# Performance work log

Measured on AMD Instinct MI355X. Metric: run time of the kernel, lower is better.

## Reference

```python
import jax, jax.numpy as jnp
import numpy as np

DIM = 1024
SEQ_LEN = 4096
K = 256
HEADS = 16
DIM_HEAD = DIM // HEADS  # 64
BATCH = 4


def setup_inputs() -> dict:
    key = jax.random.key(0)
    ks = jax.random.split(key, 8)
    x = jax.random.normal(ks[0], (BATCH, SEQ_LEN, DIM), dtype=jnp.float32)
    # nn.Linear weights are [out, in]; y = x @ W.T
    std_lin = 1.0 / np.sqrt(DIM)
    Wq = jax.random.uniform(ks[1], (HEADS * DIM_HEAD, DIM), minval=-std_lin, maxval=std_lin, dtype=jnp.float32)
    Wk = jax.random.uniform(ks[2], (HEADS * DIM_HEAD, DIM), minval=-std_lin, maxval=std_lin, dtype=jnp.float32)
    Wv = jax.random.uniform(ks[3], (HEADS * DIM_HEAD, DIM), minval=-std_lin, maxval=std_lin, dtype=jnp.float32)
    # proj_k/proj_v init_: uniform(-1/sqrt(k), 1/sqrt(k)) on [seq_len, k]
    std_p = 1.0 / np.sqrt(K)
    proj_k = jax.random.uniform(ks[4], (SEQ_LEN, K), minval=-std_p, maxval=std_p, dtype=jnp.float32)
    proj_v = jax.random.uniform(ks[5], (SEQ_LEN, K), minval=-std_p, maxval=std_p, dtype=jnp.float32)
    std_o = 1.0 / np.sqrt(HEADS * DIM_HEAD)
    Wo = jax.random.uniform(ks[6], (DIM, HEADS * DIM_HEAD), minval=-std_o, maxval=std_o, dtype=jnp.float32)
    bo = jax.random.uniform(ks[7], (DIM,), minval=-std_o, maxval=std_o, dtype=jnp.float32)
    return {"x": x, "Wq": Wq, "Wk": Wk, "Wv": Wv, "proj_k": proj_k, "proj_v": proj_v, "Wo": Wo, "bo": bo}


def reference(x, Wq, Wk, Wv, proj_k, proj_v, Wo, bo):
    b, n, d = x.shape
    h, dh, k = HEADS, DIM_HEAD, K
    # q/k/v projections
    q = jnp.einsum('bnd,ed->bne', x, Wq)            # [b, n, h*dh]
    keys = jnp.einsum('bnd,ed->bne', x, Wk)         # [b, n, h*dh]
    vals = jnp.einsum('bnd,ed->bne', x, Wv)         # [b, n, h*dh]
    # low-rank projection along sequence: [b, n, e] x [n, k] -> [b, k, e]
    keys = jnp.einsum('bne,nk->bke', keys, proj_k[:n])
    vals = jnp.einsum('bne,nk->bke', vals, proj_v[:n])
    # split heads
    q = q.reshape(b, n, h, dh).transpose(0, 2, 1, 3)        # [b, h, n, dh]
    keys = keys.reshape(b, k, h, dh).transpose(0, 2, 1, 3)  # [b, h, k, dh]
    vals = vals.reshape(b, k, h, dh).transpose(0, 2, 1, 3)  # [b, h, k, dh]
    dots = jnp.einsum('bhnd,bhkd->bhnk', q, keys) * (dh ** -0.5)
    attn = jax.nn.softmax(dots, axis=-1)
    out = jnp.einsum('bhnk,bhkd->bhnd', attn, vals)
    out = out.transpose(0, 2, 1, 3).reshape(b, n, h * dh)
    return jnp.einsum('bne,oe->bno', out, Wo) + bo
```

## Files before the change

### kernel.cpp

```cpp
#include <hip/hip_runtime.h>
#include <hip/hip_bf16.h>
#include <stdint.h>

typedef unsigned short u16;
typedef __attribute__((ext_vector_type(8))) short bf16x8;
typedef __attribute__((ext_vector_type(4))) float f32x4;

#define DEV __device__ __forceinline__

DEV u16 f2bf(float f) {
  union { float f; unsigned u; } v; v.f = f;
  unsigned r = (v.u + 0x7fffu + ((v.u >> 16) & 1u)) >> 16;
  return (u16)r;
}

DEV float bf2f(u16 h) {
  union { unsigned u; float f; } v; v.u = ((unsigned)h) << 16;
  return v.f;
}

DEV unsigned pk2(float lo, float hi) {
  union { __hip_bfloat162 h; unsigned u; } c;
  c.h = __float22bfloat162_rn(make_float2(lo, hi));
  return c.u;
}

DEV f32x4 mfma16(bf16x8 a, bf16x8 b, f32x4 c) {
  return __builtin_amdgcn_mfma_f32_16x16x32_bf16(a, b, c, 0, 0, 0);
}

DEV void gload_lds16(const u16* g, u16* l) {
  __builtin_amdgcn_global_load_lds((const __attribute__((address_space(1))) void*)g,
                                   (__attribute__((address_space(3))) void*)l, 16, 0, 0);
}

#define QSCALE 0.18033688011112042f

__global__ void cvt_xpose_kernel(const float* __restrict__ src, u16* __restrict__ dst_rm,
                                 u16* __restrict__ dst_tp, int R, int C,
                                 long zS, long zRM, long zTP) {
  __shared__ u16 tile[64][72];
  src += (size_t)blockIdx.z * zS;
  dst_tp += (size_t)blockIdx.z * zTP;
  int r0 = blockIdx.y * 64, c0 = blockIdx.x * 64;
  int tr = threadIdx.x >> 2, tc = (threadIdx.x & 3) * 16;
  const float* s = src + (size_t)(r0 + tr) * C + c0 + tc;
  u16 loc[16];
#pragma unroll
  for (int q = 0; q < 4; ++q) {
    float4 v = ((const float4*)s)[q];
    loc[q * 4 + 0] = f2bf(v.x); loc[q * 4 + 1] = f2bf(v.y);
    loc[q * 4 + 2] = f2bf(v.z); loc[q * 4 + 3] = f2bf(v.w);
  }
#pragma unroll
  for (int i = 0; i < 16; ++i) tile[tr][tc + i] = loc[i];
  if (dst_rm) {
    u16* d = dst_rm + (size_t)blockIdx.z * zRM + (size_t)(r0 + tr) * C + c0 + tc;
    *(bf16x8*)d = *(const bf16x8*)&loc[0];
    *(bf16x8*)(d + 8) = *(const bf16x8*)&loc[8];
  }
  __syncthreads();
  u16 tmp[16];
#pragma unroll
  for (int i = 0; i < 16; ++i) tmp[i] = tile[tc + i][tr];
  u16* d = dst_tp + (size_t)(c0 + tr) * R + r0 + tc;
  *(bf16x8*)d = *(const bf16x8*)&tmp[0];
  *(bf16x8*)(d + 8) = *(const bf16x8*)&tmp[8];
}

__global__ void cvt_misc_kernel(const float* __restrict__ s0, const float* __restrict__ s1,
                                const float* __restrict__ s2, const float* __restrict__ s3,
                                u16* __restrict__ d0, u16* __restrict__ d1,
                                u16* __restrict__ d2, u16* __restrict__ d3,
                                const float* __restrict__ pk, const float* __restrict__ pv,
                                u16* __restrict__ projT) {
  __shared__ u16 tile[64][72];
  const int y = blockIdx.y;
  if (y < 4) {
    const float* s; u16* d;
    switch (y) {
      case 0: s = s0; d = d0; break;
      case 1: s = s1; d = d1; break;
      case 2: s = s2; d = d2; break;
      default: s = s3; d = d3; break;
    }
    int i = blockIdx.x * 256 + threadIdx.x;
    float4 v = ((const float4*)s)[i];
    ushort4 o; o.x = f2bf(v.x); o.y = f2bf(v.y); o.z = f2bf(v.z); o.w = f2bf(v.w);
    ((ushort4*)d)[i] = o;
    return;
  }
  if (blockIdx.x >= 256) return;
  const float* src = (y == 4) ? pk : pv;
  u16* dst = projT + (size_t)(y - 4) * 1048576;
  int r0 = (blockIdx.x >> 2) * 64, c0 = (blockIdx.x & 3) * 64;
  int tr = threadIdx.x >> 2, tc = (threadIdx.x & 3) * 16;
  const float* s = src + (size_t)(r0 + tr) * 256 + c0 + tc;
  u16 loc[16];
#pragma unroll
  for (int q = 0; q < 4; ++q) {
    float4 v = ((const float4*)s)[q];
    loc[q * 4 + 0] = f2bf(v.x); loc[q * 4 + 1] = f2bf(v.y);
    loc[q * 4 + 2] = f2bf(v.z); loc[q * 4 + 3] = f2bf(v.w);
  }
#pragma unroll
  for (int i = 0; i < 16; ++i) tile[tr][tc + i] = loc[i];
  __syncthreads();
  u16 tmp[16];
#pragma unroll
  for (int i = 0; i < 16; ++i) tmp[i] = tile[tc + i][tr];
  u16* d = dst + (size_t)(c0 + tr) * 4096 + r0 + tc;
  *(bf16x8*)d = *(const bf16x8*)&tmp[0];
  *(bf16x8*)(d + 8) = *(const bf16x8*)&tmp[8];
}

__global__ void reduce4_kernel(const u16* __restrict__ part, u16* __restrict__ out) {
  int i = blockIdx.x * 256 + threadIdx.x;
  bf16x8 a = ((const bf16x8*)part)[i];
  bf16x8 b = ((const bf16x8*)part)[i + 262144];
  bf16x8 c = ((const bf16x8*)part)[i + 524288];
  bf16x8 d = ((const bf16x8*)part)[i + 786432];
  u16 o[8];
#pragma unroll
  for (int j = 0; j < 8; ++j)
    o[j] = f2bf(bf2f((u16)a[j]) + bf2f((u16)b[j]) + bf2f((u16)c[j]) + bf2f((u16)d[j]));
  ((bf16x8*)out)[i] = *(const bf16x8*)&o[0];
}

template<int OMODE>
__global__ __launch_bounds__(256, 4)
void gemm_bt_kernel(const u16* __restrict__ A, const u16* __restrict__ Bt,
                    const u16* __restrict__ Bt2, void* __restrict__ Cout,
                    u16* __restrict__ CoutT, const float* __restrict__ bias, float cscale,
                    int ldA, int ldB, int ldC, int Klen,
                    long zA, long zB, long zC, int bMod, long kChunkA, long kChunkB) {
  __shared__ __align__(16) u16 smA[2][128 * 32];
  __shared__ __align__(16) u16 smB[2][128 * 32];
  const int t = threadIdx.x;
  const int lane = t & 63, wave = t >> 6;
  const int wm = wave & 1, wn = wave >> 1;
  const int g = lane >> 4, r = lane & 15;
  const int id = blockIdx.y * gridDim.x + blockIdx.x;
  const int cpx = (gridDim.x * gridDim.y) >> 3;
  const int s = (id & 7) * cpx + (id >> 3);
  const int bx = s % gridDim.x, by = s / gridDim.x;
  const int z = blockIdx.z;
  const int b = z % bMod, kc = z / bMod;
  const u16* Ab = A + (size_t)b * zA + (size_t)kc * kChunkA;
  const u16* Bbase = (Bt2 && (b & 1)) ? Bt2 : Bt;
  const u16* Bb = Bbase + (size_t)b * zB + (size_t)kc * kChunkB;
  const int m0 = by * 128, n0 = bx * 128;
  const int srow = t >> 2;
  const int lslot = ((t & 3) + 4 - ((srow >> 1) & 3)) & 3;

  f32x4 acc[4][4];
#pragma unroll
  for (int m = 0; m < 4; ++m)
#pragma unroll
    for (int n = 0; n < 4; ++n) acc[m][n] = f32x4{0.f, 0.f, 0.f, 0.f};

  auto STAGE = [&](int buf, int k0) {
#pragma unroll
    for (int p = 0; p < 2; ++p) {
      int row = p * 64 + srow;
      gload_lds16(Ab + (size_t)(m0 + row) * ldA + k0 + lslot * 8, &smA[buf][p * 2048 + wave * 512]);
      gload_lds16(Bb + (size_t)(n0 + row) * ldB + k0 + lslot * 8, &smB[buf][p * 2048 + wave * 512]);
    }
  };

  const int nt = Klen >> 5;
  STAGE(0, 0);
  __syncthreads();
  int cur = 0;
  for (int it = 0; it < nt; ++it) {
    if (it + 1 < nt) STAGE(cur ^ 1, (it + 1) << 5);
    bf16x8 af[4], bfr[4];
#pragma unroll
    for (int m = 0; m < 4; ++m) {
      int row = wm * 64 + m * 16 + r;
      int ps = (g + (row >> 1)) & 3;
      af[m] = *(const bf16x8*)&smA[cur][row * 32 + ps * 8];
    }
#pragma unroll
    for (int n = 0; n < 4; ++n) {
      int row = wn * 64 + n * 16 + r;
      int ps = (g + (row >> 1)) & 3;
      bfr[n] = *(const bf16x8*)&smB[cur][row * 32 + ps * 8];
    }
#pragma unroll
    for (int m = 0; m < 4; ++m)
#pragma unroll
      for (int n = 0; n < 4; ++n)
        acc[m][n] = mfma16(af[m], bfr[n], acc[m][n]);
    __syncthreads();
    cur ^= 1;
  }

  if constexpr (OMODE == 4) {
    u16* myT = (u16*)&smA[0][0] + wave * 4096;
    u16* Cg = (u16*)Cout + (size_t)z * zC + (size_t)(m0 + wm * 64) * ldC + n0 + wn * 64;
#pragma unroll
    for (int m = 0; m < 4; ++m)
#pragma unroll
      for (int n = 0; n < 4; ++n)
#pragma unroll
        for (int rr = 0; rr < 4; ++rr) {
          int rl = m * 16 + 4 * g + rr;
          int cl = n * 16 + r;
          myT[rl * 64 + (((cl >> 3) ^ (rl & 7)) << 3) + (cl & 7)] = f2bf(acc[m][n][rr]);
        }
#pragma unroll
    for (int i = 0; i < 8; ++i) {
      int idx = i * 64 + lane;
      int row = idx >> 3, c8 = idx & 7;
      bf16x8 v = *(const bf16x8*)&myT[row * 64 + ((c8 ^ (row & 7)) << 3)];
      *(bf16x8*)&Cg[(size_t)row * ldC + c8 * 8] = v;
    }
  } else {
    if ((z & 1) == 0) {
      u16* C = (u16*)Cout + (size_t)(z >> 1) * zC;
#pragma unroll
      for (int n = 0; n < 4; ++n) {
        int col = n0 + wn * 64 + n * 16 + r;
#pragma unroll
        for (int m = 0; m < 4; ++m) {
          int rowb = m0 + wm * 64 + m * 16 + 4 * g;
#pragma unroll
          for (int rr = 0; rr < 4; ++rr)
            C[(size_t)(rowb + rr) * ldC + col] = f2bf(acc[m][n][rr]);
        }
      }
    } else {
      u16* C = CoutT + (size_t)(z >> 1) * zC;
#pragma unroll
      for (int n = 0; n < 4; ++n) {
        int col = n0 + wn * 64 + n * 16 + r;
#pragma unroll
        for (int m = 0; m < 4; ++m) {
          int rowb = m0 + wm * 64 + m * 16 + 4 * g;
          ushort4 o;
          o.x = f2bf(acc[m][n][0]); o.y = f2bf(acc[m][n][1]);
          o.z = f2bf(acc[m][n][2]); o.w = f2bf(acc[m][n][3]);
          *(ushort4*)&C[(size_t)col * 256 + rowb] = o;
        }
      }
    }
  }
}

template<int OMODE>
__global__ __launch_bounds__(512, 4)
void qgemm128_kernel(const u16* __restrict__ A, const u16* __restrict__ Bt,
                     void* __restrict__ Cout, const float* __restrict__ bias,
                     float cscale, int ldA, int ldB, int ldC, int Klen) {
  __shared__ __align__(16) u16 lds[36864];
  const int t = threadIdx.x;
  const int lane = t & 63, wave = t >> 6;
  const int g = lane >> 4, r = lane & 15;
  const int wm = wave >> 2, wn = wave & 3;
  const int id = blockIdx.y * gridDim.x + blockIdx.x;
  const int cpx = (gridDim.x * gridDim.y) >> 3;
  const int s = (id & 7) * cpx + (id >> 3);
  const int bx = s & 3, by = s >> 2;
  const int m0 = by * 128, n0 = bx * 256;

  const int srow = t >> 2;
  const int lslot = ((t & 3) + 4 - ((srow >> 1) & 3)) & 3;

  auto STAGE = [&](int buf, int k0) {
    gload_lds16(A + (size_t)(m0 + srow) * ldA + k0 + lslot * 8,
                lds + buf * 4096 + t * 8);
#pragma unroll
    for (int p = 0; p < 2; ++p)
      gload_lds16(Bt + (size_t)(n0 + p * 128 + srow) * ldB + k0 + lslot * 8,
                  lds + 12288 + buf * 8192 + p * 4096 + t * 8);
  };

  f32x4 acc[4][4];
#pragma unroll
  for (int m = 0; m < 4; ++m)
#pragma unroll
    for (int n = 0; n < 4; ++n) acc[m][n] = f32x4{0.f, 0.f, 0.f, 0.f};

  const int nt = Klen >> 5;
  STAGE(0, 0);
  STAGE(1, 32);
  asm volatile("s_waitcnt vmcnt(3)" ::: "memory");
  __builtin_amdgcn_s_barrier();

  int cur = 0;
  for (int it = 0; it < nt; ++it) {
    int pre = cur + 2; if (pre >= 3) pre -= 3;
    if (it + 2 < nt) STAGE(pre, (it + 2) << 5);
    const u16* Ab = lds + cur * 4096;
    const u16* Bb = lds + 12288 + cur * 8192;
    bf16x8 af[4], bfr[4];
#pragma unroll
    for (int m = 0; m < 4; ++m) {
      int row = wm * 64 + m * 16 + r;
      int ps = (g + (row >> 1)) & 3;
      af[m] = *(const bf16x8*)&Ab[row * 32 + ps * 8];
    }
#pragma unroll
    for (int n = 0; n < 4; ++n) {
      int row = wn * 64 + n * 16 + r;
      int ps = (g + (row >> 1)) & 3;
      bfr[n] = *(const bf16x8*)&Bb[row * 32 + ps * 8];
    }
#pragma unroll
    for (int m = 0; m < 4; ++m)
#pragma unroll
      for (int n = 0; n < 4; ++n)
        acc[m][n] = mfma16(af[m], bfr[n], acc[m][n]);
    if (it + 1 < nt) {
      if (it + 2 < nt) asm volatile("s_waitcnt vmcnt(3)" ::: "memory");
      else             asm volatile("s_waitcnt vmcnt(0)" ::: "memory");
      __builtin_amdgcn_s_barrier();
    }
    cur = cur + 1; if (cur >= 3) cur -= 3;
  }
  __builtin_amdgcn_s_barrier();

  if constexpr (OMODE == 0) {
    u16* myT = lds + wave * 2048;
    u16* Cg = (u16*)Cout + (size_t)(m0 + wm * 64) * ldC + n0 + wn * 64;
#pragma unroll
    for (int np = 0; np < 2; ++np) {
#pragma unroll
      for (int n2 = 0; n2 < 2; ++n2)
#pragma unroll
        for (int m = 0; m < 4; ++m)
#pragma unroll
          for (int rr = 0; rr < 4; ++rr) {
            int rl = m * 16 + 4 * g + rr;
            int cl = n2 * 16 + r;
            myT[rl * 32 + (((cl >> 3) ^ (rl & 3)) << 3) + (cl & 7)] =
                f2bf(acc[m][np * 2 + n2][rr] * cscale);
          }
#pragma unroll
      for (int i = 0; i < 4; ++i) {
        int idx = i * 64 + lane;
        int row = idx >> 2, c = idx & 3;
        bf16x8 v = *(const bf16x8*)&myT[row * 32 + ((c ^ (row & 3)) << 3)];
        *(bf16x8*)&Cg[(size_t)row * ldC + np * 32 + c * 8] = v;
      }
    }
  } else {
    float* myF = (float*)lds + wave * 2048;
    float bvn[4];
#pragma unroll
    for (int n = 0; n < 4; ++n) bvn[n] = bias[n0 + wn * 64 + n * 16 + r];
    float* Cg = (float*)Cout + (size_t)(m0 + wm * 64) * ldC + n0 + wn * 64;
#pragma unroll
    for (int np = 0; np < 2; ++np) {
#pragma unroll
      for (int n2 = 0; n2 < 2; ++n2)
#pragma unroll
        for (int m = 0; m < 4; ++m)
#pragma unroll
          for (int rr = 0; rr < 4; ++rr) {
            int rl = m * 16 + 4 * g + rr;
            int cl = n2 * 16 + r;
            myF[rl * 32 + ((((cl >> 2) ^ (rl & 7)) & 7) << 2) + (cl & 3)] =
                acc[m][np * 2 + n2][rr] + bvn[np * 2 + n2];
          }
#pragma unroll
      for (int i = 0; i < 8; ++i) {
        int idx = i * 64 + lane;
        int row = idx >> 3, c = idx & 7;
        float4 v = *(const float4*)&myF[row * 32 + (((c ^ (row & 7)) & 7) << 2)];
        *(float4*)&Cg[(size_t)row * ldC + np * 32 + c * 4] = v;
      }
    }
  }
}

__global__ __launch_bounds__(256, 3)
void attn_kernel(const u16* __restrict__ Q, const u16* __restrict__ Kl,
                 const u16* __restrict__ VT, u16* __restrict__ Out) {
  __shared__ __align__(16) u16 sm[24576];
  const int t = threadIdx.x, lane = t & 63, w = t >> 6;
  const int g = lane >> 4, r = lane & 15;
  const int id = (blockIdx.y << 6) | blockIdx.x;
  const int s = (id & 7) * (gridDim.y << 3) + (id >> 3);
  const int b = blockIdx.z, h = s >> 6, n0 = (s & 63) * 64;
  const u16* Kb = Kl + (size_t)b * 262144 + h * 64;
  const u16* Vb = VT + (size_t)b * 262144 + (size_t)(h * 64) * 256;
  u16* vbase = sm + 16384;

  auto stage_slice = [&](int sl64, int buf) {
#pragma unroll
    for (int i = 0; i < 2; ++i) {
      int u = i * 256 + t;
      int d = u >> 3, ps = u & 7;
      gload_lds16(Vb + (size_t)d * 256 + sl64 * 64 + (ps ^ (d & 7)) * 8,
                  vbase + buf * 4096 + i * 2048 + t * 8);
    }
  };

#pragma unroll
  for (int p = 0; p < 8; ++p) {
    int row = p * 32 + (t >> 3);
    int ls = ((t & 7) + 8 - (row & 7)) & 7;
    gload_lds16(Kb + (size_t)row * 1024 + ls * 8, sm + p * 2048 + w * 512);
  }
  stage_slice(0, 0);
  stage_slice(1, 1);
  const int qrow = n0 + w * 16 + r;
  const u16* Qp = Q + ((size_t)(b * 4096 + qrow)) * 1024 + h * 64 + g * 8;
  bf16x8 aq0 = *(const bf16x8*)Qp;
  bf16x8 aq1 = *(const bf16x8*)(Qp + 32);
  asm volatile("s_waitcnt vmcnt(4)" ::: "memory");
  __builtin_amdgcn_s_barrier();

  f32x4 dotv[16];
  __builtin_amdgcn_s_setprio(1);
#pragma unroll
  for (int kf = 0; kf < 16; ++kf) {
    int row = kf * 16 + r;
    bf16x8 kb0 = *(const bf16x8*)&sm[row * 64 + ((g + row) & 7) * 8];
    bf16x8 kb1 = *(const bf16x8*)&sm[row * 64 + ((4 + g + row) & 7) * 8];
    f32x4 d = f32x4{0.f, 0.f, 0.f, 0.f};
    d = mfma16(kb0, aq0, d);
    d = mfma16(kb1, aq1, d);
    dotv[kf] = d;
  }
  __builtin_amdgcn_s_setprio(0);
  asm volatile("s_waitcnt vmcnt(2)" ::: "memory");
  __builtin_amdgcn_s_barrier();

  float mx = -3.4e38f;
#pragma unroll
  for (int kf = 0; kf < 16; ++kf)
    mx = fmaxf(mx, fmaxf(fmaxf(dotv[kf][0], dotv[kf][1]), fmaxf(dotv[kf][2], dotv[kf][3])));
  mx = fmaxf(mx, __shfl_xor(mx, 16, 64));
  mx = fmaxf(mx, __shfl_xor(mx, 32, 64));
  float ssum = 0.f;
#pragma unroll
  for (int kf = 0; kf < 16; ++kf)
#pragma unroll
    for (int j = 0; j < 4; ++j) {
      float p = __builtin_amdgcn_exp2f(dotv[kf][j] - mx);
      dotv[kf][j] = p;
      ssum += p;
    }
  ssum += __shfl_xor(ssum, 16, 64);
  ssum += __shfl_xor(ssum, 32, 64);
  const float inv = 1.f / ssum;
  float invv[4];
#pragma unroll
  for (int rr = 0; rr < 4; ++rr) invv[rr] = __shfl(inv, 4 * g + rr, 64);

  const int q16 = w * 16 + r;
  const int qx = (q16 & 7) << 3;
#pragma unroll
  for (int kf = 0; kf < 16; ++kf) {
    uint2 val;
    val.x = pk2(dotv[kf][0], dotv[kf][1]);
    val.y = pk2(dotv[kf][2], dotv[kf][3]);
    *(uint2*)&sm[(q16 * 256 + kf * 16 + 4 * g) ^ qx] = val;
  }

  f32x4 oacc[4];
#pragma unroll
  for (int df = 0; df < 4; ++df) oacc[df] = f32x4{0.f, 0.f, 0.f, 0.f};
#pragma unroll
  for (int ph = 0; ph < 4; ++ph) {
    const u16* vb = vbase + (ph & 1) * 4096;
    __builtin_amdgcn_s_setprio(1);
#pragma unroll
    for (int kk2 = 0; kk2 < 2; ++kk2) {
      int kk = ph * 2 + kk2;
      bf16x8 ap = *(const bf16x8*)&sm[(q16 * 256 + kk * 32 + g * 8) ^ qx];
#pragma unroll
      for (int df = 0; df < 4; ++df) {
        int d = df * 16 + r;
        bf16x8 bv = *(const bf16x8*)&vb[d * 64 + ((kk2 * 4 + g) ^ (d & 7)) * 8];
        oacc[df] = mfma16(ap, bv, oacc[df]);
      }
    }
    __builtin_amdgcn_s_setprio(0);
    if (ph < 3) {
      asm volatile("s_waitcnt vmcnt(0)" ::: "memory");
      __builtin_amdgcn_s_barrier();
      if (ph < 2) stage_slice(ph + 2, ph & 1);
    }
  }

  u16* myO = sm + w * 4096;
#pragma unroll
  for (int df = 0; df < 4; ++df)
#pragma unroll
    for (int rr = 0; rr < 4; ++rr) {
      int row = 4 * g + rr;
      int col = df * 16 + r;
      myO[row * 64 + (((col >> 3) ^ (row & 7)) << 3) + (col & 7)] = f2bf(oacc[df][rr] * invv[rr]);
    }
#pragma unroll
  for (int i = 0; i < 2; ++i) {
    int idx = i * 64 + lane;
    int row = idx >> 3, c8 = idx & 7;
    bf16x8 v = *(const bf16x8*)&myO[row * 64 + ((c8 ^ (row & 7)) << 3)];
    *(bf16x8*)&Out[((size_t)(b * 4096 + n0 + w * 16 + row)) * 1024 + h * 64 + c8 * 8] = v;
  }
}

extern "C" void kernel_launch(void* const* d_in, const int* in_sizes, int n_in,
                              void* d_out, int out_size, void* d_ws, size_t ws_size,
                              hipStream_t stream) {
  const float* x  = (const float*)d_in[0];
  const float* Wq = (const float*)d_in[1];
  const float* Wk = (const float*)d_in[2];
  const float* Wv = (const float*)d_in[3];
  const float* pk = (const float*)d_in[4];
  const float* pv = (const float*)d_in[5];
  const float* Wo = (const float*)d_in[6];
  const float* bo = (const float*)d_in[7];

  u16* ws = (u16*)d_ws;
  u16* xbf   = ws;
  u16* xT    = xbf + 16777216;
  u16* wqb   = xT + 16777216;
  u16* wkb   = wqb + 1048576;
  u16* wvb   = wkb + 1048576;
  u16* wob   = wvb + 1048576;
  u16* projT = wob + 1048576;
  u16* Qb    = projT + 2097152;
  u16* xp    = Qb + 16777216;
  u16* klow  = xp + 2097152;
  u16* vT    = klow + 1048576;
  u16* aout  = xbf;
  u16* xp_part = Qb;

  cvt_xpose_kernel<<<dim3(16, 64, 4), 256, 0, stream>>>(x, xbf, xT, 4096, 1024,
                                                        4194304, 4194304, 4194304);
  cvt_misc_kernel<<<dim3(1024, 6), 256, 0, stream>>>(Wq, Wk, Wv, Wo, wqb, wkb, wvb, wob,
                                                     pk, pv, projT);
  gemm_bt_kernel<4><<<dim3(32, 4, 4), 256, 0, stream>>>(
      projT, xT, nullptr, (void*)xp_part, nullptr, nullptr, 1.f,
      4096, 4096, 4096, 1024, 0, 0, 2097152, 1, 1024, 1024);
  reduce4_kernel<<<1024, 256, 0, stream>>>(xp_part, xp);
  gemm_bt_kernel<3><<<dim3(8, 2, 8), 256, 0, stream>>>(
      xp, wkb, wvb, (void*)klow, vT, nullptr, 1.f,
      4096, 1024, 1024, 1024, 1048576, 0, 262144, 2, 1024, 0);
  qgemm128_kernel<0><<<dim3(4, 128), 512, 0, stream>>>(
      xbf, wqb, (void*)Qb, nullptr, QSCALE, 1024, 1024, 1024, 1024);
  attn_kernel<<<dim3(64, 16, 4), 256, 0, stream>>>(Qb, klow, vT, aout);
  qgemm128_kernel<1><<<dim3(4, 128), 512, 0, stream>>>(
      aout, wob, d_out, bo, 1.f, 1024, 1024, 1024, 1024);
}
```

Baseline: 205.5 us.

## Retile Q and output GEMMs to 128x128 blocks with 64-deep double-buffered K

Replaces the 512-thread 128x256-tile GEMM with a 256-thread 128x128-tile version. Each step now stages 64 K elements into two buffers, replacing the three buffers of 32 used before, with an 8-slot rotated swizzle. The bf16 epilogue writes a full 64x64 wave tile through LDS in one pass. The aim is more, smaller blocks for better CU balance and fewer barrier iterations. The cost is less operand reuse per block and a shallower prefetch pipeline.

```diff
diff --git a/kernel.cpp b/kernel.cpp
--- a/kernel.cpp
+++ b/kernel.cpp
@@ -249,31 +249,38 @@
 }
 
 template<int OMODE>
-__global__ __launch_bounds__(512, 4)
-void qgemm128_kernel(const u16* __restrict__ A, const u16* __restrict__ Bt,
-                     void* __restrict__ Cout, const float* __restrict__ bias,
-                     float cscale, int ldA, int ldB, int ldC, int Klen) {
-  __shared__ __align__(16) u16 lds[36864];
+__global__ __launch_bounds__(256, 2)
+void qgemm64_kernel(const u16* __restrict__ A, const u16* __restrict__ Bt,
+                    void* __restrict__ Cout, const float* __restrict__ bias,
+                    float cscale, int ldA, int ldB, int ldC, int Klen) {
+  __shared__ __align__(16) u16 lds[32768];
   const int t = threadIdx.x;
   const int lane = t & 63, wave = t >> 6;
   const int g = lane >> 4, r = lane & 15;
-  const int wm = wave >> 2, wn = wave & 3;
+  const int wm = wave >> 1, wn = wave & 1;
   const int id = blockIdx.y * gridDim.x + blockIdx.x;
   const int cpx = (gridDim.x * gridDim.y) >> 3;
   const int s = (id & 7) * cpx + (id >> 3);
-  const int bx = s & 3, by = s >> 2;
-  const int m0 = by * 128, n0 = bx * 256;
-
-  const int srow = t >> 2;
-  const int lslot = ((t & 3) + 4 - ((srow >> 1) & 3)) & 3;
+  const int bx = s & 7, by = s >> 3;
+  const int m0 = by * 128, n0 = bx * 128;
 
   auto STAGE = [&](int buf, int k0) {
-    gload_lds16(A + (size_t)(m0 + srow) * ldA + k0 + lslot * 8,
-                lds + buf * 4096 + t * 8);
-#pragma unroll
-    for (int p = 0; p < 2; ++p)
-      gload_lds16(Bt + (size_t)(n0 + p * 128 + srow) * ldB + k0 + lslot * 8,
-                  lds + 12288 + buf * 8192 + p * 4096 + t * 8);
+#pragma unroll
+    for (int j = 0; j < 4; ++j) {
+      int u = j * 256 + t;
+      int row = u >> 3, psl = u & 7;
+      int sl = (psl + 8 - (row & 7)) & 7;
+      gload_lds16(A + (size_t)(m0 + row) * ldA + k0 + sl * 8,
+                  lds + buf * 16384 + u * 8);
+    }
+#pragma unroll
+    for (int j = 0; j < 4; ++j) {
+      int u = j * 256 + t;
+      int row = u >> 3, psl = u & 7;
+      int sl = (psl + 8 - (row & 7)) & 7;
+      gload_lds16(Bt + (size_t)(n0 + row) * ldB + k0 + sl * 8,
+                  lds + buf * 16384 + 8192 + u * 8);
+    }
   };
 
   f32x4 acc[4][4];
@@ -282,68 +289,63 @@
 #pragma unroll
     for (int n = 0; n < 4; ++n) acc[m][n] = f32x4{0.f, 0.f, 0.f, 0.f};
 
-  const int nt = Klen >> 5;
+  const int nt = Klen >> 6;
   STAGE(0, 0);
-  STAGE(1, 32);
-  asm volatile("s_waitcnt vmcnt(3)" ::: "memory");
+  asm volatile("s_waitcnt vmcnt(0)" ::: "memory");
   __builtin_amdgcn_s_barrier();
 
   int cur = 0;
   for (int it = 0; it < nt; ++it) {
-    int pre = cur + 2; if (pre >= 3) pre -= 3;
-    if (it + 2 < nt) STAGE(pre, (it + 2) << 5);
-    const u16* Ab = lds + cur * 4096;
-    const u16* Bb = lds + 12288 + cur * 8192;
-    bf16x8 af[4], bfr[4];
+    if (it + 1 < nt) STAGE(cur ^ 1, (it + 1) << 6);
+    const u16* Ab = lds + cur * 16384;
+    const u16* Bb = Ab + 8192;
+    bf16x8 af[4][2], bfr[4][2];
 #pragma unroll
     for (int m = 0; m < 4; ++m) {
       int row = wm * 64 + m * 16 + r;
-      int ps = (g + (row >> 1)) & 3;
-      af[m] = *(const bf16x8*)&Ab[row * 32 + ps * 8];
+      af[m][0] = *(const bf16x8*)&Ab[row * 64 + (((g + row) & 7) << 3)];
+      af[m][1] = *(const bf16x8*)&Ab[row * 64 + (((4 + g + row) & 7) << 3)];
     }
 #pragma unroll
     for (int n = 0; n < 4; ++n) {
       int row = wn * 64 + n * 16 + r;
-      int ps = (g + (row >> 1)) & 3;
-      bfr[n] = *(const bf16x8*)&Bb[row * 32 + ps * 8];
+      bfr[n][0] = *(const bf16x8*)&Bb[row * 64 + (((g + row) & 7) << 3)];
+      bfr[n][1] = *(const bf16x8*)&Bb[row * 64 + (((4 + g + row) & 7) << 3)];
     }
 #pragma unroll
     for (int m = 0; m < 4; ++m)
 #pragma unroll
+      for (int n = 0; n < 4; ++n) {
+        acc[m][n] = mfma16(af[m][0], bfr[n][0], acc[m][n]);
+        acc[m][n] = mfma16(af[m][1], bfr[n][1], acc[m][n]);
+      }
+    if (it + 1 < nt) {
+      asm volatile("s_waitcnt vmcnt(0)" ::: "memory");
+      __builtin_amdgcn_s_barrier();
+    }
+    cur ^= 1;
+  }
+  __builtin_amdgcn_s_barrier();
+
+  if constexpr (OMODE == 0) {
+    u16* myT = lds + wave * 4096;
+    u16* Cg = (u16*)Cout + (size_t)(m0 + wm * 64) * ldC + n0 + wn * 64;
+#pragma unroll
+    for (int m = 0; m < 4; ++m)
+#pragma unroll
       for (int n = 0; n < 4; ++n)
-        acc[m][n] = mfma16(af[m], bfr[n], acc[m][n]);
-    if (it + 1 < nt) {
-      if (it + 2 < nt) asm volatile("s_waitcnt vmcnt(3)" ::: "memory");
-      else             asm volatile("s_waitcnt vmcnt(0)" ::: "memory");
-      __builtin_amdgcn_s_barrier();
-    }
-    cur = cur + 1; if (cur >= 3) cur -= 3;
-  }
-  __builtin_amdgcn_s_barrier();
-
-  if constexpr (OMODE == 0) {
-    u16* myT = lds + wave * 2048;
-    u16* Cg = (u16*)Cout + (size_t)(m0 + wm * 64) * ldC + n0 + wn * 64;
-#pragma unroll
-    for (int np = 0; np < 2; ++np) {
-#pragma unroll
-      for (int n2 = 0; n2 < 2; ++n2)
-#pragma unroll
-        for (int m = 0; m < 4; ++m)
-#pragma unroll
-          for (int rr = 0; rr < 4; ++rr) {
-            int rl = m * 16 + 4 * g + rr;
-            int cl = n2 * 16 + r;
-            myT[rl * 32 + (((cl >> 3) ^ (rl & 3)) << 3) + (cl & 7)] =
-                f2bf(acc[m][np * 2 + n2][rr] * cscale);
-          }
-#pragma unroll
-      for (int i = 0; i < 4; ++i) {
-        int idx = i * 64 + lane;
-        int row = idx >> 2, c = idx & 3;
-        bf16x8 v = *(const bf16x8*)&myT[row * 32 + ((c ^ (row & 3)) << 3)];
-        *(bf16x8*)&Cg[(size_t)row * ldC + np * 32 + c * 8] = v;
-      }
+#pragma unroll
+        for (int rr = 0; rr < 4; ++rr) {
+          int rl = m * 16 + 4 * g + rr;
+          int cl = n * 16 + r;
+          myT[rl * 64 + (((cl >> 3) ^ (rl & 7)) << 3) + (cl & 7)] = f2bf(acc[m][n][rr] * cscale);
+        }
+#pragma unroll
+    for (int i = 0; i < 8; ++i) {
+      int idx = i * 64 + lane;
+      int row = idx >> 3, c8 = idx & 7;
+      bf16x8 v = *(const bf16x8*)&myT[row * 64 + ((c8 ^ (row & 7)) << 3)];
+      *(bf16x8*)&Cg[(size_t)row * ldC + c8 * 8] = v;
     }
   } else {
     float* myF = (float*)lds + wave * 2048;
@@ -543,9 +545,9 @@
   gemm_bt_kernel<3><<<dim3(8, 2, 8), 256, 0, stream>>>(
       xp, wkb, wvb, (void*)klow, vT, nullptr, 1.f,
       4096, 1024, 1024, 1024, 1048576, 0, 262144, 2, 1024, 0);
-  qgemm128_kernel<0><<<dim3(4, 128), 512, 0, stream>>>(
+  qgemm64_kernel<0><<<dim3(8, 128), 256, 0, stream>>>(
       xbf, wqb, (void*)Qb, nullptr, QSCALE, 1024, 1024, 1024, 1024);
   attn_kernel<<<dim3(64, 16, 4), 256, 0, stream>>>(Qb, klow, vT, aout);
-  qgemm128_kernel<1><<<dim3(4, 128), 512, 0, stream>>>(
+  qgemm64_kernel<1><<<dim3(8, 128), 256, 0, stream>>>(
       aout, wob, d_out, bo, 1.f, 1024, 1024, 1024, 1024);
 }
```

Result: no change. 201.7 us (-1.9%).
